# Optimization experiments

Measured on AMD Instinct MI355X. Metric: run time of the kernel, lower is better.

## Reference

```python
import jax, jax.numpy as jnp
import numpy as np

DIM = 256
NUM_HEADS = 8
HEAD_DIM = DIM // NUM_HEADS  # 32
DILATIONS = (1, 2, 4, 8)
ND = len(DILATIONS)          # 4
K = 3                        # kernel_size
KK = K * K                   # 9
SCALE = HEAD_DIM ** -0.5
LN_EPS = 1e-5


def _unfold(t, dil, k=K):
    # t: (B, d, H, W) -> (B, d, k*k, H, W); same-size dilated im2col (stride 1,
    # padding dil*(k-1)//2), kernel positions in row-major order like nn.Unfold.
    B, d, H, W = t.shape
    p = dil * (k - 1) // 2
    tp = jnp.pad(t, ((0, 0), (0, 0), (p, p), (p, p)))
    patches = [tp[:, :, i * dil:i * dil + H, j * dil:j * dil + W]
               for i in range(k) for j in range(k)]
    return jnp.stack(patches, axis=2)


def setup_inputs() -> dict:
    key = jax.random.key(0)
    ks = jax.random.split(key, 10)
    B, C, H, W = 8, DIM, 64, 64
    s = lambda fan: fan ** -0.5
    return {
        "x": jax.random.normal(ks[0], (B, C, H, W), jnp.float32),
        "qkv_w": jax.random.normal(ks[1], (3 * C, C), jnp.float32) * s(C),
        "qkv_b": jnp.zeros((3 * C,), jnp.float32),
        "fc_w": jax.random.normal(ks[2], (ND, ND), jnp.float32) * s(ND),
        "fc_b": jnp.zeros((ND,), jnp.float32),
        "ln_g": jnp.ones((C // ND,), jnp.float32),
        "ln_b": jnp.zeros((C // ND,), jnp.float32),
        "proj_w": jax.random.normal(ks[3], (C, C), jnp.float32) * s(C),
        "proj_b": jnp.zeros((C,), jnp.float32),
    }


def reference(x, qkv_w, qkv_b, fc_w, fc_b, ln_g, ln_b, proj_w, proj_b):
    B, C, H, W = x.shape
    d = C // ND            # channels per dilation branch
    h = d // HEAD_DIM      # heads per branch
    L = H * W

    # 1x1 conv qkv: (B, 3C, H, W) -> (B, 3, ND, d, H, W)
    qkv = jnp.einsum('bchw,oc->bohw', x, qkv_w) + qkv_b[None, :, None, None]
    qkv = qkv.reshape(B, 3, ND, d, H, W)

    feats = []
    for i, dil in enumerate(DILATIONS):
        q = qkv[:, 0, i]                                # (B, d, H, W)
        kmap = qkv[:, 1, i]
        vmap = qkv[:, 2, i]
        qr = q.reshape(B, h, HEAD_DIM, L)               # (B, h, hd, L)
        ku = _unfold(kmap, dil).reshape(B, h, HEAD_DIM, KK, L)
        vu = _unfold(vmap, dil).reshape(B, h, HEAD_DIM, KK, L)
        # per-pixel window attention: scores (B, h, L, KK)
        attn = jnp.einsum('bhcl,bhcpl->bhlp', qr, ku) * SCALE
        attn = jax.nn.softmax(attn, axis=-1)
        out = jnp.einsum('bhlp,bhcpl->bhlc', attn, vu)  # (B, h, L, hd)
        feats.append(out.transpose(0, 2, 1, 3).reshape(B, H, W, d))

    # Cross-scale fusion: mix the S=ND scale axis with a small linear layer
    stacked = jnp.stack(feats, axis=3)                  # (B, H, W, S, d)
    fused = jnp.einsum('bhwsc,ts->bhwtc', stacked, fc_w) \
        + fc_b[None, None, None, :, None]
    fused = fused + stacked
    mu = fused.mean(axis=-1, keepdims=True)
    var = fused.var(axis=-1, keepdims=True)
    fused = (fused - mu) * jax.lax.rsqrt(var + LN_EPS) * ln_g + ln_b

    y2 = fused.reshape(B, H, W, C)
    y3 = y2 @ proj_w.T + proj_b
    return y3.transpose(0, 3, 1, 2)                     # (B, C, H, W)
```

## Files before the change

### kernel.cpp

```cpp
#include <hip/hip_runtime.h>
#include <stdint.h>

typedef __attribute__((ext_vector_type(8))) short bf16x8;
typedef __attribute__((ext_vector_type(4))) float f32x4;
typedef _Float16 h2 __attribute__((ext_vector_type(2)));

#define AS1 __attribute__((address_space(1)))
#define AS3 __attribute__((address_space(3)))

__device__ __forceinline__ void gload_lds16(const void* g, void* l){
  __builtin_amdgcn_global_load_lds((AS1 void*)g, (AS3 void*)l, 16, 0, 0);
}

__device__ __forceinline__ unsigned short to_bf16(float f){
  union { float f; unsigned int i; } x; x.f = f;
  unsigned int u = x.i;
  unsigned int r = (u + 0x7fffu + ((u >> 16) & 1u)) >> 16;
  return (unsigned short)r;
}
__device__ __forceinline__ unsigned short to_f16(float f){
  _Float16 h = (_Float16)f;
  return __builtin_bit_cast(unsigned short, h);
}
__device__ __forceinline__ float bf2f(unsigned short s){
  union { unsigned int i; float f; } x; x.i = ((unsigned int)s) << 16; return x.f;
}

union HU { uint4 u; h2 h[4]; };

__device__ __forceinline__ float dpp_qsum(float v){
  int a  = __builtin_bit_cast(int, v);
  int p1 = __builtin_amdgcn_update_dpp(0, a, 0xB1, 0xF, 0xF, true);
  float s = v + __builtin_bit_cast(float, p1);
  int c  = __builtin_bit_cast(int, s);
  int p2 = __builtin_amdgcn_update_dpp(0, c, 0x4E, 0xF, 0xF, true);
  return s + __builtin_bit_cast(float, p2);
}

__device__ __forceinline__ float wave_sum64(float v){
  int x;
  x = __builtin_amdgcn_update_dpp(0, __builtin_bit_cast(int, v), 0x111, 0xF, 0xF, true);
  v += __builtin_bit_cast(float, x);
  x = __builtin_amdgcn_update_dpp(0, __builtin_bit_cast(int, v), 0x112, 0xF, 0xF, true);
  v += __builtin_bit_cast(float, x);
  x = __builtin_amdgcn_update_dpp(0, __builtin_bit_cast(int, v), 0x114, 0xF, 0xF, true);
  v += __builtin_bit_cast(float, x);
  x = __builtin_amdgcn_update_dpp(0, __builtin_bit_cast(int, v), 0x118, 0xF, 0xF, true);
  v += __builtin_bit_cast(float, x);
  x = __builtin_amdgcn_update_dpp(0, __builtin_bit_cast(int, v), 0x142, 0xF, 0xF, true);
  v += __builtin_bit_cast(float, x);
  x = __builtin_amdgcn_update_dpp(0, __builtin_bit_cast(int, v), 0x143, 0xF, 0xF, true);
  v += __builtin_bit_cast(float, x);
  return __builtin_bit_cast(float, __builtin_amdgcn_readlane(__builtin_bit_cast(int, v), 63));
}

__device__ __forceinline__ float dot8(const h2* q, const h2* k, float acc){
#if __has_builtin(__builtin_amdgcn_fdot2)
  #pragma unroll
  for (int g = 0; g < 4; g++) acc = __builtin_amdgcn_fdot2(q[g], k[g], acc, false);
#else
  #pragma unroll
  for (int g = 0; g < 4; g++)
    acc += (float)q[g][0] * (float)k[g][0] + (float)q[g][1] * (float)k[g][1];
#endif
  return acc;
}

__global__ __launch_bounds__(256) void prep_kernel(const float* __restrict__ x,
                                                   unsigned short* __restrict__ xb,
                                                   const float* __restrict__ qkv_w,
                                                   const float* __restrict__ proj_w,
                                                   unsigned short* __restrict__ wq,
                                                   unsigned short* __restrict__ wp){
  int bid = blockIdx.x;
  int tid = threadIdx.x;
  if (bid >= 2048){
    int i = (bid - 2048) * 256 + tid;
    const int nq4 = 768 * 256 / 4;
    const int np4 = 256 * 256 / 4;
    if (i < nq4){
      float4 v = ((const float4*)qkv_w)[i];
      ushort4 u; u.x = to_bf16(v.x); u.y = to_bf16(v.y); u.z = to_bf16(v.z); u.w = to_bf16(v.w);
      ((ushort4*)wq)[i] = u;
    } else if (i < nq4 + np4){
      float4 v = ((const float4*)proj_w)[i - nq4];
      ushort4 u; u.x = to_bf16(v.x); u.y = to_bf16(v.y); u.z = to_bf16(v.z); u.w = to_bf16(v.w);
      ((ushort4*)wp)[i - nq4] = u;
    }
    return;
  }
  __shared__ float tile[64][65];
  int l0 = (bid & 63) * 64;
  int c0 = ((bid >> 6) & 3) * 64;
  int b  = bid >> 8;
  const float* xp = x + ((size_t)b * 256 + c0) * 4096 + l0;
  #pragma unroll
  for (int rep = 0; rep < 4; rep++){
    int idx = rep * 256 + tid;
    int cl = idx >> 4, q4 = idx & 15;
    float4 v = *(const float4*)(xp + (size_t)cl * 4096 + q4 * 4);
    tile[cl][q4 * 4 + 0] = v.x;
    tile[cl][q4 * 4 + 1] = v.y;
    tile[cl][q4 * 4 + 2] = v.z;
    tile[cl][q4 * 4 + 3] = v.w;
  }
  __syncthreads();
  unsigned short* op = xb + ((size_t)b * 4096 + l0) * 256 + c0;
  #pragma unroll
  for (int rep = 0; rep < 4; rep++){
    int idx = rep * 256 + tid;
    int ll = idx >> 4, cp = (idx & 15) * 4;
    ushort4 u;
    u.x = to_bf16(tile[cp + 0][ll]);
    u.y = to_bf16(tile[cp + 1][ll]);
    u.z = to_bf16(tile[cp + 2][ll]);
    u.w = to_bf16(tile[cp + 3][ll]);
    *(ushort4*)(op + (size_t)ll * 256 + cp) = u;
  }
}

__device__ __forceinline__ void stage_tile(const unsigned short* __restrict__ A,
                                           const unsigned short* __restrict__ B,
                                           unsigned short* la, unsigned short* lb,
                                           int tid, int wave, int k0){
  #pragma unroll
  for (int inst = 0; inst < 4; inst++){
    int u    = inst * 256 + tid;
    int row  = u >> 3;
    int col  = u & 7;
    int scol = col ^ (row & 7);
    gload_lds16(A + (size_t)row * 256 + k0 + scol * 8, la + inst * 2048 + wave * 512);
    gload_lds16(B + (size_t)row * 256 + k0 + scol * 8, lb + inst * 2048 + wave * 512);
  }
}

__device__ __forceinline__ void compute_tile(const unsigned short* la, const unsigned short* lb,
                                             int lane, int m_w, int n_w, f32x4 acc[4][4]){
  #pragma unroll
  for (int kk = 0; kk < 2; kk++){
    bf16x8 ar[4], br[4];
    int slot = kk * 4 + (lane >> 4);
    #pragma unroll
    for (int i = 0; i < 4; i++){
      int rowa = m_w + i * 16 + (lane & 15);
      ar[i] = *(const bf16x8*)((const char*)la + rowa * 128 + ((slot ^ (rowa & 7)) << 4));
      int rowb = n_w + i * 16 + (lane & 15);
      br[i] = *(const bf16x8*)((const char*)lb + rowb * 128 + ((slot ^ (rowb & 7)) << 4));
    }
    #pragma unroll
    for (int i = 0; i < 4; i++){
      #pragma unroll
      for (int j = 0; j < 4; j++)
        acc[i][j] = __builtin_amdgcn_mfma_f32_16x16x32_bf16(ar[i], br[j], acc[i][j], 0, 0, 0);
    }
  }
}

__global__ __launch_bounds__(256, 2) void qkv_gemm_kernel(
    const unsigned short* __restrict__ Wq, const unsigned short* __restrict__ xb,
    const float* __restrict__ qkv_b, unsigned short* __restrict__ qkv){
  __shared__ __align__(16) unsigned short lA[2][128 * 64];
  __shared__ __align__(16) unsigned short lB[2][128 * 64];
  int orig   = blockIdx.x;
  int b      = orig & 7;
  int tile   = orig >> 3;
  int tile_m = tile % 6;
  int tile_n = tile / 6;
  int tid  = threadIdx.x;
  int lane = tid & 63;
  int wave = tid >> 6;
  int m_w = (wave >> 1) * 64;
  int n_w = (wave & 1) * 64;

  f32x4 zero; zero[0]=0.f; zero[1]=0.f; zero[2]=0.f; zero[3]=0.f;
  f32x4 acc[4][4];
  #pragma unroll
  for (int i = 0; i < 4; i++)
    #pragma unroll
    for (int j = 0; j < 4; j++) acc[i][j] = zero;

  const unsigned short* Abase = Wq + (size_t)tile_m * 128 * 256;
  const unsigned short* Bbase = xb + ((size_t)b * 4096 + (size_t)tile_n * 128) * 256;

  stage_tile(Abase, Bbase, lA[0], lB[0], tid, wave, 0);
  __syncthreads();
  #pragma unroll
  for (int ks = 0; ks < 4; ks++){
    int cur = ks & 1, nxt = cur ^ 1;
    if (ks < 3) stage_tile(Abase, Bbase, lA[nxt], lB[nxt], tid, wave, (ks + 1) * 64);
    compute_tile(lA[cur], lB[cur], lane, m_w, n_w, acc);
    if (ks < 3) __syncthreads();
  }

  #pragma unroll
  for (int i = 0; i < 4; i++){
    #pragma unroll
    for (int j = 0; j < 4; j++){
      int l  = tile_n * 128 + n_w + j * 16 + (lane & 15);
      int o0 = tile_m * 128 + m_w + i * 16 + ((lane >> 4) << 2);
      ushort4 u;
      u.x = to_f16(acc[i][j][0] + qkv_b[o0 + 0]);
      u.y = to_f16(acc[i][j][1] + qkv_b[o0 + 1]);
      u.z = to_f16(acc[i][j][2] + qkv_b[o0 + 2]);
      u.w = to_f16(acc[i][j][3] + qkv_b[o0 + 3]);
      *(ushort4*)(qkv + ((size_t)(b * 24 + (o0 >> 5)) * 4096 + l) * 32 + (o0 & 31)) = u;
    }
  }
}

__global__ __launch_bounds__(256, 4) void attn_fcln_kernel(
    const unsigned short* __restrict__ qkv,
    const float* __restrict__ fc_w, const float* __restrict__ fc_b,
    const float* __restrict__ ln_g, const float* __restrict__ ln_b,
    unsigned short* __restrict__ y2){
  __shared__ float fsm[16 * 260];
  int tid  = threadIdx.x;
  int orig = blockIdx.x;
  int b    = orig & 7;
  int l0   = (orig >> 3) * 16;
  int lc   = tid & 3;
  int px   = (tid >> 2) & 15;
  int di   = tid >> 6;
  int dil  = 1 << di;
  int l    = l0 + px;
  int yy = l >> 6, xx = l & 63;

  int cidx[9]; bool ib[9];
  #pragma unroll
  for (int p = 0; p < 9; p++){
    int ny = yy + (p / 3 - 1) * dil;
    int nx = xx + (p % 3 - 1) * dil;
    ib[p] = ((unsigned)ny < 64u) && ((unsigned)nx < 64u);
    int nyc = min(max(ny, 0), 63);
    int nxc = min(max(nx, 0), 63);
    cidx[p] = nyc * 64 + nxc;
  }

  #pragma unroll
  for (int head = 0; head < 2; head++){
    const unsigned short* qp = qkv + ((size_t)(b * 24 +      di * 2 + head) * 4096 + l) * 32 + lc * 8;
    const unsigned short* kb = qkv + ((size_t)(b * 24 +  8 + di * 2 + head) * 4096) * 32;
    const unsigned short* vb = qkv + ((size_t)(b * 24 + 16 + di * 2 + head) * 4096) * 32;

    HU qu; qu.u = *(const uint4*)qp;
    HU ku[9], vu[9];
    #pragma unroll
    for (int p = 0; p < 9; p++)
      ku[p].u = *(const uint4*)(kb + (size_t)cidx[p] * 32 + lc * 8);
    #pragma unroll
    for (int p = 0; p < 9; p++)
      vu[p].u = *(const uint4*)(vb + (size_t)cidx[p] * 32 + lc * 8);

    float sc[9];
    #pragma unroll
    for (int p = 0; p < 9; p++){
      float part = dot8(qu.h, ku[p].h, 0.f);
      float s = dpp_qsum(part) * 0.17677669529663687f;
      sc[p] = ib[p] ? s : 0.f;
    }
    float mx = sc[0];
    #pragma unroll
    for (int p = 1; p < 9; p++) mx = fmaxf(mx, sc[p]);
    float w[9]; float den = 0.f;
    #pragma unroll
    for (int p = 0; p < 9; p++){ w[p] = __expf(sc[p] - mx); den += w[p]; }
    float inv = 1.f / den;

    h2 o2[4];
    #pragma unroll
    for (int g = 0; g < 4; g++){ o2[g][0] = (_Float16)0.f; o2[g][1] = (_Float16)0.f; }
    #pragma unroll
    for (int p = 0; p < 9; p++){
      float wpf = ib[p] ? (w[p] * inv) : 0.f;
      _Float16 wh = (_Float16)wpf;
      h2 w2; w2[0] = wh; w2[1] = wh;
      #pragma unroll
      for (int g = 0; g < 4; g++) o2[g] += w2 * vu[p].h[g];
    }
    float* fp = fsm + px * 260 + di * 64 + head * 32 + lc * 8;
    #pragma unroll
    for (int g = 0; g < 4; g++){
      fp[g * 2 + 0] = (float)o2[g][0];
      fp[g * 2 + 1] = (float)o2[g][1];
    }
  }
  __syncthreads();

  int c  = tid & 63;
  int wv = tid >> 6;
  float g  = ln_g[c], bb = ln_b[c];
  float fw[4][4], fb[4];
  #pragma unroll
  for (int t = 0; t < 4; t++){
    fb[t] = fc_b[t];
    #pragma unroll
    for (int s = 0; s < 4; s++) fw[t][s] = fc_w[t * 4 + s];
  }
  #pragma unroll
  for (int pp = 0; pp < 4; pp++){
    int p = wv * 4 + pp;
    float st[4];
    #pragma unroll
    for (int s = 0; s < 4; s++) st[s] = fsm[p * 260 + s * 64 + c];
    unsigned short* op = y2 + ((size_t)(b * 4096) + l0 + p) * 256;
    #pragma unroll
    for (int t = 0; t < 4; t++){
      float v = fb[t] + st[t];
      #pragma unroll
      for (int s = 0; s < 4; s++) v += fw[t][s] * st[s];
      float s1 = wave_sum64(v);
      float s2 = wave_sum64(v * v);
      float mu  = s1 * 0.015625f;
      float var = s2 * 0.015625f - mu * mu;
      float rs  = rsqrtf(var + 1e-5f);
      op[t * 64 + c] = to_bf16((v - mu) * rs * g + bb);
    }
  }
}

__global__ __launch_bounds__(256, 2) void proj_gemm_kernel(
    const unsigned short* __restrict__ Wp, const unsigned short* __restrict__ y2,
    const float* __restrict__ proj_b, float* __restrict__ out){
  __shared__ __align__(16) unsigned short lA[2][128 * 64];
  __shared__ __align__(16) unsigned short lB[2][128 * 64];
  int orig   = blockIdx.x;
  int b      = orig & 7;
  int tile   = orig >> 3;
  int tile_m = tile & 1;
  int tile_n = tile >> 1;
  int tid  = threadIdx.x;
  int lane = tid & 63;
  int wave = tid >> 6;
  int m_w = (wave >> 1) * 64;
  int n_w = (wave & 1) * 64;

  f32x4 zero; zero[0]=0.f; zero[1]=0.f; zero[2]=0.f; zero[3]=0.f;
  f32x4 acc[4][4];
  #pragma unroll
  for (int i = 0; i < 4; i++)
    #pragma unroll
    for (int j = 0; j < 4; j++) acc[i][j] = zero;

  const unsigned short* Abase = Wp + (size_t)tile_m * 128 * 256;
  const unsigned short* Bbase = y2 + ((size_t)b * 4096 + (size_t)tile_n * 128) * 256;

  stage_tile(Abase, Bbase, lA[0], lB[0], tid, wave, 0);
  __syncthreads();
  #pragma unroll
  for (int ks = 0; ks < 4; ks++){
    int cur = ks & 1, nxt = cur ^ 1;
    if (ks < 3) stage_tile(Abase, Bbase, lA[nxt], lB[nxt], tid, wave, (ks + 1) * 64);
    compute_tile(lA[cur], lB[cur], lane, m_w, n_w, acc);
    if (ks < 3) __syncthreads();
  }

  #pragma unroll
  for (int i = 0; i < 4; i++){
    #pragma unroll
    for (int j = 0; j < 4; j++){
      int l = tile_n * 128 + n_w + j * 16 + (lane & 15);
      #pragma unroll
      for (int r = 0; r < 4; r++){
        int o = tile_m * 128 + m_w + i * 16 + ((lane >> 4) << 2) + r;
        out[((size_t)b * 256 + o) * 4096 + l] = acc[i][j][r] + proj_b[o];
      }
    }
  }
}

extern "C" void kernel_launch(void* const* d_in, const int* in_sizes, int n_in,
                              void* d_out, int out_size, void* d_ws, size_t ws_size,
                              hipStream_t stream){
  const float* x      = (const float*)d_in[0];
  const float* qkv_w  = (const float*)d_in[1];
  const float* qkv_b  = (const float*)d_in[2];
  const float* fc_w   = (const float*)d_in[3];
  const float* fc_b   = (const float*)d_in[4];
  const float* ln_g   = (const float*)d_in[5];
  const float* ln_b   = (const float*)d_in[6];
  const float* proj_w = (const float*)d_in[7];
  const float* proj_b = (const float*)d_in[8];
  float* out = (float*)d_out;

  unsigned short* xb  = (unsigned short*)d_ws;
  unsigned short* qkv = xb  + (size_t)8 * 4096 * 256;
  unsigned short* wq  = qkv + (size_t)8 * 24 * 4096 * 32;
  unsigned short* wp  = wq  + (size_t)768 * 256;
  unsigned short* y2  = xb;

  hipLaunchKernelGGL(prep_kernel,      dim3(2304), dim3(256), 0, stream, x, xb, qkv_w, proj_w, wq, wp);
  hipLaunchKernelGGL(qkv_gemm_kernel,  dim3(1536), dim3(256), 0, stream, wq, xb, qkv_b, qkv);
  hipLaunchKernelGGL(attn_fcln_kernel, dim3(2048), dim3(256), 0, stream, qkv, fc_w, fc_b, ln_g, ln_b, y2);
  hipLaunchKernelGGL(proj_gemm_kernel, dim3(512),  dim3(256), 0, stream, wp, y2, proj_b, out);
}
```

Before: 68.23 us.

## Fuse x transpose/bf16 cast into QKV GEMM B-tile loading; add nontemporal hints

Removes the prep pass that transposed x into a bf16 channel-last buffer. The QKV GEMM now reads fp32 x directly through registers, converts it to bf16 and writes swizzled B tiles into LDS, so the intermediate write and reread of x are avoided. Weight casting moves to a small separate kernel. Nontemporal loads and stores are added for q, y2 and the output. The trade-off is that the GEMM is re-reading x for each of its 6 M tiles in fp32, twice the bytes of bf16, and its B staging now goes through registers instead of direct global-to-LDS loads.

New measurement: 75.97 us. 1.11x slower.

```diff
diff --git a/kernel.cpp b/kernel.cpp
--- a/kernel.cpp
+++ b/kernel.cpp
@@ -4,6 +4,7 @@
 typedef __attribute__((ext_vector_type(8))) short bf16x8;
 typedef __attribute__((ext_vector_type(4))) float f32x4;
 typedef _Float16 h2 __attribute__((ext_vector_type(2)));
+typedef unsigned int u32x4 __attribute__((ext_vector_type(4)));
 
 #define AS1 __attribute__((address_space(1)))
 #define AS3 __attribute__((address_space(3)))
@@ -22,11 +23,8 @@
   _Float16 h = (_Float16)f;
   return __builtin_bit_cast(unsigned short, h);
 }
-__device__ __forceinline__ float bf2f(unsigned short s){
-  union { unsigned int i; float f; } x; x.i = ((unsigned int)s) << 16; return x.f;
-}
-
-union HU { uint4 u; h2 h[4]; };
+
+union HU { u32x4 u; h2 h[4]; };
 
 __device__ __forceinline__ float dpp_qsum(float v){
   int a  = __builtin_bit_cast(int, v);
@@ -66,56 +64,31 @@
   return acc;
 }
 
-__global__ __launch_bounds__(256) void prep_kernel(const float* __restrict__ x,
-                                                   unsigned short* __restrict__ xb,
-                                                   const float* __restrict__ qkv_w,
-                                                   const float* __restrict__ proj_w,
-                                                   unsigned short* __restrict__ wq,
-                                                   unsigned short* __restrict__ wp){
-  int bid = blockIdx.x;
-  int tid = threadIdx.x;
-  if (bid >= 2048){
-    int i = (bid - 2048) * 256 + tid;
-    const int nq4 = 768 * 256 / 4;
-    const int np4 = 256 * 256 / 4;
-    if (i < nq4){
-      float4 v = ((const float4*)qkv_w)[i];
-      ushort4 u; u.x = to_bf16(v.x); u.y = to_bf16(v.y); u.z = to_bf16(v.z); u.w = to_bf16(v.w);
-      ((ushort4*)wq)[i] = u;
-    } else if (i < nq4 + np4){
-      float4 v = ((const float4*)proj_w)[i - nq4];
-      ushort4 u; u.x = to_bf16(v.x); u.y = to_bf16(v.y); u.z = to_bf16(v.z); u.w = to_bf16(v.w);
-      ((ushort4*)wp)[i - nq4] = u;
-    }
-    return;
-  }
-  __shared__ float tile[64][65];
-  int l0 = (bid & 63) * 64;
-  int c0 = ((bid >> 6) & 3) * 64;
-  int b  = bid >> 8;
-  const float* xp = x + ((size_t)b * 256 + c0) * 4096 + l0;
-  #pragma unroll
-  for (int rep = 0; rep < 4; rep++){
-    int idx = rep * 256 + tid;
-    int cl = idx >> 4, q4 = idx & 15;
-    float4 v = *(const float4*)(xp + (size_t)cl * 4096 + q4 * 4);
-    tile[cl][q4 * 4 + 0] = v.x;
-    tile[cl][q4 * 4 + 1] = v.y;
-    tile[cl][q4 * 4 + 2] = v.z;
-    tile[cl][q4 * 4 + 3] = v.w;
-  }
-  __syncthreads();
-  unsigned short* op = xb + ((size_t)b * 4096 + l0) * 256 + c0;
-  #pragma unroll
-  for (int rep = 0; rep < 4; rep++){
-    int idx = rep * 256 + tid;
-    int ll = idx >> 4, cp = (idx & 15) * 4;
-    ushort4 u;
-    u.x = to_bf16(tile[cp + 0][ll]);
-    u.y = to_bf16(tile[cp + 1][ll]);
-    u.z = to_bf16(tile[cp + 2][ll]);
-    u.w = to_bf16(tile[cp + 3][ll]);
-    *(ushort4*)(op + (size_t)ll * 256 + cp) = u;
+__global__ void cast_w_kernel(const float* __restrict__ qkv_w, const float* __restrict__ proj_w,
+                              unsigned short* __restrict__ wq, unsigned short* __restrict__ wp){
+  int i = blockIdx.x * 256 + threadIdx.x;
+  const int nq4 = 768 * 256 / 4;
+  const int np4 = 256 * 256 / 4;
+  if (i < nq4){
+    float4 v = ((const float4*)qkv_w)[i];
+    ushort4 u; u.x = to_bf16(v.x); u.y = to_bf16(v.y); u.z = to_bf16(v.z); u.w = to_bf16(v.w);
+    ((ushort4*)wq)[i] = u;
+  } else if (i < nq4 + np4){
+    float4 v = ((const float4*)proj_w)[i - nq4];
+    ushort4 u; u.x = to_bf16(v.x); u.y = to_bf16(v.y); u.z = to_bf16(v.z); u.w = to_bf16(v.w);
+    ((ushort4*)wp)[i - nq4] = u;
+  }
+}
+
+__device__ __forceinline__ void stage_a(const unsigned short* __restrict__ A,
+                                        unsigned short* la, int tid, int wave, int k0){
+  #pragma unroll
+  for (int inst = 0; inst < 4; inst++){
+    int u    = inst * 256 + tid;
+    int row  = u >> 3;
+    int col  = u & 7;
+    int scol = col ^ (row & 7);
+    gload_lds16(A + (size_t)row * 256 + k0 + scol * 8, la + inst * 2048 + wave * 512);
   }
 }
 
@@ -156,8 +129,35 @@
   }
 }
 
+__device__ __forceinline__ void bload_x(const float* __restrict__ xsrc, int k0, int l0,
+                                        int tid, float bf[4][8]){
+  int w  = tid >> 6, ln = tid & 63;
+  int ll = (w & 1) * 64 + ln;
+  int sb = (w >> 1) * 4;
+  const float* col = xsrc + (size_t)(k0 + sb * 8) * 4096 + l0 + ll;
+  #pragma unroll
+  for (int i = 0; i < 4; i++)
+    #pragma unroll
+    for (int j = 0; j < 8; j++)
+      bf[i][j] = col[(size_t)(i * 8 + j) * 4096];
+}
+__device__ __forceinline__ void bwrite_x(unsigned short* lb, int tid, const float bf[4][8]){
+  int w  = tid >> 6, ln = tid & 63;
+  int ll = (w & 1) * 64 + ln;
+  int sb = (w >> 1) * 4;
+  #pragma unroll
+  for (int i = 0; i < 4; i++){
+    int slot = sb + i;
+    bf16x8 v;
+    #pragma unroll
+    for (int j = 0; j < 8; j++)
+      ((unsigned short*)&v)[j] = to_bf16(bf[i][j]);
+    *(bf16x8*)((char*)lb + ll * 128 + ((slot ^ (ll & 7)) << 4)) = v;
+  }
+}
+
 __global__ __launch_bounds__(256, 2) void qkv_gemm_kernel(
-    const unsigned short* __restrict__ Wq, const unsigned short* __restrict__ xb,
+    const unsigned short* __restrict__ Wq, const float* __restrict__ x,
     const float* __restrict__ qkv_b, unsigned short* __restrict__ qkv){
   __shared__ __align__(16) unsigned short lA[2][128 * 64];
   __shared__ __align__(16) unsigned short lB[2][128 * 64];
@@ -171,6 +171,7 @@
   int wave = tid >> 6;
   int m_w = (wave >> 1) * 64;
   int n_w = (wave & 1) * 64;
+  int l0  = tile_n * 128;
 
   f32x4 zero; zero[0]=0.f; zero[1]=0.f; zero[2]=0.f; zero[3]=0.f;
   f32x4 acc[4][4];
@@ -180,23 +181,32 @@
     for (int j = 0; j < 4; j++) acc[i][j] = zero;
 
   const unsigned short* Abase = Wq + (size_t)tile_m * 128 * 256;
-  const unsigned short* Bbase = xb + ((size_t)b * 4096 + (size_t)tile_n * 128) * 256;
-
-  stage_tile(Abase, Bbase, lA[0], lB[0], tid, wave, 0);
+  const float* xsrc = x + (size_t)b * 256 * 4096;
+
+  float bf[4][8];
+  bload_x(xsrc, 0, l0, tid, bf);
+  stage_a(Abase, lA[0], tid, wave, 0);
+  bwrite_x(lB[0], tid, bf);
   __syncthreads();
   #pragma unroll
   for (int ks = 0; ks < 4; ks++){
     int cur = ks & 1, nxt = cur ^ 1;
-    if (ks < 3) stage_tile(Abase, Bbase, lA[nxt], lB[nxt], tid, wave, (ks + 1) * 64);
+    if (ks < 3){
+      bload_x(xsrc, (ks + 1) * 64, l0, tid, bf);
+      stage_a(Abase, lA[nxt], tid, wave, (ks + 1) * 64);
+    }
     compute_tile(lA[cur], lB[cur], lane, m_w, n_w, acc);
-    if (ks < 3) __syncthreads();
+    if (ks < 3){
+      bwrite_x(lB[nxt], tid, bf);
+      __syncthreads();
+    }
   }
 
   #pragma unroll
   for (int i = 0; i < 4; i++){
     #pragma unroll
     for (int j = 0; j < 4; j++){
-      int l  = tile_n * 128 + n_w + j * 16 + (lane & 15);
+      int l  = l0 + n_w + j * 16 + (lane & 15);
       int o0 = tile_m * 128 + m_w + i * 16 + ((lane >> 4) << 2);
       ushort4 u;
       u.x = to_f16(acc[i][j][0] + qkv_b[o0 + 0]);
@@ -242,14 +252,14 @@
     const unsigned short* kb = qkv + ((size_t)(b * 24 +  8 + di * 2 + head) * 4096) * 32;
     const unsigned short* vb = qkv + ((size_t)(b * 24 + 16 + di * 2 + head) * 4096) * 32;
 
-    HU qu; qu.u = *(const uint4*)qp;
+    HU qu; qu.u = __builtin_nontemporal_load((const u32x4*)qp);
     HU ku[9], vu[9];
     #pragma unroll
     for (int p = 0; p < 9; p++)
-      ku[p].u = *(const uint4*)(kb + (size_t)cidx[p] * 32 + lc * 8);
+      ku[p].u = *(const u32x4*)(kb + (size_t)cidx[p] * 32 + lc * 8);
     #pragma unroll
     for (int p = 0; p < 9; p++)
-      vu[p].u = *(const uint4*)(vb + (size_t)cidx[p] * 32 + lc * 8);
+      vu[p].u = *(const u32x4*)(vb + (size_t)cidx[p] * 32 + lc * 8);
 
     float sc[9];
     #pragma unroll
@@ -313,7 +323,7 @@
       float mu  = s1 * 0.015625f;
       float var = s2 * 0.015625f - mu * mu;
       float rs  = rsqrtf(var + 1e-5f);
-      op[t * 64 + c] = to_bf16((v - mu) * rs * g + bb);
+      __builtin_nontemporal_store(to_bf16((v - mu) * rs * g + bb), op + t * 64 + c);
     }
   }
 }
@@ -362,7 +372,8 @@
       #pragma unroll
       for (int r = 0; r < 4; r++){
         int o = tile_m * 128 + m_w + i * 16 + ((lane >> 4) << 2) + r;
-        out[((size_t)b * 256 + o) * 4096 + l] = acc[i][j][r] + proj_b[o];
+        __builtin_nontemporal_store(acc[i][j][r] + proj_b[o],
+                                    out + ((size_t)b * 256 + o) * 4096 + l);
       }
     }
   }
@@ -382,14 +393,13 @@
   const float* proj_b = (const float*)d_in[8];
   float* out = (float*)d_out;
 
-  unsigned short* xb  = (unsigned short*)d_ws;
-  unsigned short* qkv = xb  + (size_t)8 * 4096 * 256;
-  unsigned short* wq  = qkv + (size_t)8 * 24 * 4096 * 32;
+  unsigned short* qkv = (unsigned short*)d_ws;
+  unsigned short* y2  = qkv + (size_t)8 * 24 * 4096 * 32;
+  unsigned short* wq  = y2  + (size_t)8 * 4096 * 256;
   unsigned short* wp  = wq  + (size_t)768 * 256;
-  unsigned short* y2  = xb;
-
-  hipLaunchKernelGGL(prep_kernel,      dim3(2304), dim3(256), 0, stream, x, xb, qkv_w, proj_w, wq, wp);
-  hipLaunchKernelGGL(qkv_gemm_kernel,  dim3(1536), dim3(256), 0, stream, wq, xb, qkv_b, qkv);
+
+  hipLaunchKernelGGL(cast_w_kernel,    dim3(256),  dim3(256), 0, stream, qkv_w, proj_w, wq, wp);
+  hipLaunchKernelGGL(qkv_gemm_kernel,  dim3(1536), dim3(256), 0, stream, wq, x, qkv_b, qkv);
   hipLaunchKernelGGL(attn_fcln_kernel, dim3(2048), dim3(256), 0, stream, qkv, fc_w, fc_b, ln_g, ln_b, y2);
   hipLaunchKernelGGL(proj_gemm_kernel, dim3(512),  dim3(256), 0, stream, wp, y2, proj_b, out);
 }
```

## Share K/V neighbor loads across pixel pairs and use nontemporal loads/stores

Applied to the files above, without the earlier changes.

The attention kernel is restructured so each thread handles two horizontally adjacent pixels (spaced by the dilation) for a single head, instead of one pixel for both heads. The two pixels share a 3x4 tile of K/V neighbors, so each thread loads 12 vectors per tensor instead of 18 and global gather traffic drops. Query loads and the y2 and final output stores become nontemporal to reduce cache pollution. To fit the larger register footprint (24 K/V vectors held at once), launch bounds drop from 4 to 3 blocks per SIMD, which may reduce occupancy.

New measurement: 73.25 us. +7.4%, slower.

```diff
diff --git a/kernel.cpp b/kernel.cpp
--- a/kernel.cpp
+++ b/kernel.cpp
@@ -4,6 +4,7 @@
 typedef __attribute__((ext_vector_type(8))) short bf16x8;
 typedef __attribute__((ext_vector_type(4))) float f32x4;
 typedef _Float16 h2 __attribute__((ext_vector_type(2)));
+typedef unsigned int u32x4 __attribute__((ext_vector_type(4)));
 
 #define AS1 __attribute__((address_space(1)))
 #define AS3 __attribute__((address_space(3)))
@@ -22,11 +23,8 @@
   _Float16 h = (_Float16)f;
   return __builtin_bit_cast(unsigned short, h);
 }
-__device__ __forceinline__ float bf2f(unsigned short s){
-  union { unsigned int i; float f; } x; x.i = ((unsigned int)s) << 16; return x.f;
-}
-
-union HU { uint4 u; h2 h[4]; };
+
+union HU { u32x4 u; h2 h[4]; };
 
 __device__ __forceinline__ float dpp_qsum(float v){
   int a  = __builtin_bit_cast(int, v);
@@ -208,7 +206,7 @@
   }
 }
 
-__global__ __launch_bounds__(256, 4) void attn_fcln_kernel(
+__global__ __launch_bounds__(256, 3) void attn_fcln_kernel(
     const unsigned short* __restrict__ qkv,
     const float* __restrict__ fc_w, const float* __restrict__ fc_b,
     const float* __restrict__ ln_g, const float* __restrict__ ln_b,
@@ -219,69 +217,97 @@
   int b    = orig & 7;
   int l0   = (orig >> 3) * 16;
   int lc   = tid & 3;
-  int px   = (tid >> 2) & 15;
+  int pair = (tid >> 2) & 7;
+  int head = (tid >> 5) & 1;
   int di   = tid >> 6;
   int dil  = 1 << di;
-  int l    = l0 + px;
-  int yy = l >> 6, xx = l & 63;
-
-  int cidx[9]; bool ib[9];
-  #pragma unroll
-  for (int p = 0; p < 9; p++){
-    int ny = yy + (p / 3 - 1) * dil;
-    int nx = xx + (p % 3 - 1) * dil;
-    ib[p] = ((unsigned)ny < 64u) && ((unsigned)nx < 64u);
-    int nyc = min(max(ny, 0), 63);
-    int nxc = min(max(nx, 0), 63);
-    cidx[p] = nyc * 64 + nxc;
-  }
-
-  #pragma unroll
-  for (int head = 0; head < 2; head++){
-    const unsigned short* qp = qkv + ((size_t)(b * 24 +      di * 2 + head) * 4096 + l) * 32 + lc * 8;
+  int pa   = ((pair >> di) << (di + 1)) | (pair & (dil - 1));
+  int pb   = pa + dil;
+  int la   = l0 + pa;
+  int lb   = l0 + pb;
+  int yy   = la >> 6;
+  int xa   = la & 63;
+
+  int ys[3]; bool vy[3];
+  #pragma unroll
+  for (int r = 0; r < 3; r++){
+    int ny = yy + (r - 1) * dil;
+    vy[r] = ((unsigned)ny < 64u);
+    ys[r] = min(max(ny, 0), 63);
+  }
+  int xs[4]; bool vx[4];
+  #pragma unroll
+  for (int c = 0; c < 4; c++){
+    int nx = xa + (c - 1) * dil;
+    vx[c] = ((unsigned)nx < 64u);
+    xs[c] = min(max(nx, 0), 63);
+  }
+  int cidx[3][4];
+  #pragma unroll
+  for (int r = 0; r < 3; r++)
+    #pragma unroll
+    for (int c = 0; c < 4; c++)
+      cidx[r][c] = ys[r] * 64 + xs[c];
+
+  {
+    const unsigned short* qbase = qkv + ((size_t)(b * 24 +      di * 2 + head) * 4096) * 32 + lc * 8;
     const unsigned short* kb = qkv + ((size_t)(b * 24 +  8 + di * 2 + head) * 4096) * 32;
     const unsigned short* vb = qkv + ((size_t)(b * 24 + 16 + di * 2 + head) * 4096) * 32;
 
-    HU qu; qu.u = *(const uint4*)qp;
-    HU ku[9], vu[9];
-    #pragma unroll
-    for (int p = 0; p < 9; p++)
-      ku[p].u = *(const uint4*)(kb + (size_t)cidx[p] * 32 + lc * 8);
-    #pragma unroll
-    for (int p = 0; p < 9; p++)
-      vu[p].u = *(const uint4*)(vb + (size_t)cidx[p] * 32 + lc * 8);
-
-    float sc[9];
-    #pragma unroll
-    for (int p = 0; p < 9; p++){
-      float part = dot8(qu.h, ku[p].h, 0.f);
-      float s = dpp_qsum(part) * 0.17677669529663687f;
-      sc[p] = ib[p] ? s : 0.f;
-    }
-    float mx = sc[0];
-    #pragma unroll
-    for (int p = 1; p < 9; p++) mx = fmaxf(mx, sc[p]);
-    float w[9]; float den = 0.f;
-    #pragma unroll
-    for (int p = 0; p < 9; p++){ w[p] = __expf(sc[p] - mx); den += w[p]; }
-    float inv = 1.f / den;
-
-    h2 o2[4];
-    #pragma unroll
-    for (int g = 0; g < 4; g++){ o2[g][0] = (_Float16)0.f; o2[g][1] = (_Float16)0.f; }
-    #pragma unroll
-    for (int p = 0; p < 9; p++){
-      float wpf = ib[p] ? (w[p] * inv) : 0.f;
-      _Float16 wh = (_Float16)wpf;
-      h2 w2; w2[0] = wh; w2[1] = wh;
-      #pragma unroll
-      for (int g = 0; g < 4; g++) o2[g] += w2 * vu[p].h[g];
-    }
-    float* fp = fsm + px * 260 + di * 64 + head * 32 + lc * 8;
-    #pragma unroll
-    for (int g = 0; g < 4; g++){
-      fp[g * 2 + 0] = (float)o2[g][0];
-      fp[g * 2 + 1] = (float)o2[g][1];
+    HU qa, qb_;
+    qa.u  = __builtin_nontemporal_load((const u32x4*)(qbase + (size_t)la * 32));
+    qb_.u = __builtin_nontemporal_load((const u32x4*)(qbase + (size_t)lb * 32));
+    HU kt[3][4], vt[3][4];
+    #pragma unroll
+    for (int r = 0; r < 3; r++)
+      #pragma unroll
+      for (int c = 0; c < 4; c++)
+        kt[r][c].u = *(const u32x4*)(kb + (size_t)cidx[r][c] * 32 + lc * 8);
+    #pragma unroll
+    for (int r = 0; r < 3; r++)
+      #pragma unroll
+      for (int c = 0; c < 4; c++)
+        vt[r][c].u = *(const u32x4*)(vb + (size_t)cidx[r][c] * 32 + lc * 8);
+
+    #pragma unroll
+    for (int px = 0; px < 2; px++){
+      const HU& qq = px ? qb_ : qa;
+      int co = px;
+      float sc[9];
+      #pragma unroll
+      for (int p = 0; p < 9; p++){
+        int r = p / 3, cc = p % 3 + co;
+        float part = dot8(qq.h, kt[r][cc].h, 0.f);
+        float s = dpp_qsum(part) * 0.17677669529663687f;
+        sc[p] = (vy[r] && vx[cc]) ? s : 0.f;
+      }
+      float mx = sc[0];
+      #pragma unroll
+      for (int p = 1; p < 9; p++) mx = fmaxf(mx, sc[p]);
+      float w[9]; float den = 0.f;
+      #pragma unroll
+      for (int p = 0; p < 9; p++){ w[p] = __expf(sc[p] - mx); den += w[p]; }
+      float inv = 1.f / den;
+
+      h2 o2[4];
+      #pragma unroll
+      for (int g = 0; g < 4; g++){ o2[g][0] = (_Float16)0.f; o2[g][1] = (_Float16)0.f; }
+      #pragma unroll
+      for (int p = 0; p < 9; p++){
+        int r = p / 3, cc = p % 3 + co;
+        float wpf = (vy[r] && vx[cc]) ? (w[p] * inv) : 0.f;
+        _Float16 wh = (_Float16)wpf;
+        h2 w2; w2[0] = wh; w2[1] = wh;
+        #pragma unroll
+        for (int g = 0; g < 4; g++) o2[g] += w2 * vt[r][cc].h[g];
+      }
+      int pxi = px ? pb : pa;
+      float* fp = fsm + pxi * 260 + di * 64 + head * 32 + lc * 8;
+      #pragma unroll
+      for (int g = 0; g < 4; g++){
+        fp[g * 2 + 0] = (float)o2[g][0];
+        fp[g * 2 + 1] = (float)o2[g][1];
+      }
     }
   }
   __syncthreads();
@@ -313,7 +339,7 @@
       float mu  = s1 * 0.015625f;
       float var = s2 * 0.015625f - mu * mu;
       float rs  = rsqrtf(var + 1e-5f);
-      op[t * 64 + c] = to_bf16((v - mu) * rs * g + bb);
+      __builtin_nontemporal_store(to_bf16((v - mu) * rs * g + bb), op + t * 64 + c);
     }
   }
 }
@@ -362,7 +388,8 @@
       #pragma unroll
       for (int r = 0; r < 4; r++){
         int o = tile_m * 128 + m_w + i * 16 + ((lane >> 4) << 2) + r;
-        out[((size_t)b * 256 + o) * 4096 + l] = acc[i][j][r] + proj_b[o];
+        __builtin_nontemporal_store(acc[i][j][r] + proj_b[o],
+                                    out + ((size_t)b * 256 + o) * 4096 + l);
       }
     }
   }
```
